# Kernel optimization log

Measured on AMD Instinct MI355X. Metric: run time of the kernel, lower is better.

Reference implementation:

```python
import jax, jax.numpy as jnp
import numpy as np

B, S, D, H = 2, 2048, 1024, 16
DK = D // H


def setup_inputs() -> dict:
    key = jax.random.key(0)
    ks = jax.random.split(key, 11)
    scale = 1.0 / np.sqrt(D)
    inp = {
        "q": jax.random.normal(ks[0], (B, S, D), jnp.float32),
        "k": jax.random.normal(ks[1], (B, S, D), jnp.float32),
        "v": jax.random.normal(ks[2], (B, S, D), jnp.float32),
        # causal mask, broadcastable to (B, H, S, S); 0 = masked
        "mask": jnp.tril(jnp.ones((S, S), jnp.int32))[None, None, :, :],
        "wq": jax.random.normal(ks[3], (D, D), jnp.float32) * scale,
        "bq": jax.random.normal(ks[4], (D,), jnp.float32) * scale,
        "wk": jax.random.normal(ks[5], (D, D), jnp.float32) * scale,
        "bk": jax.random.normal(ks[6], (D,), jnp.float32) * scale,
        "wv": jax.random.normal(ks[7], (D, D), jnp.float32) * scale,
        "bv": jax.random.normal(ks[8], (D,), jnp.float32) * scale,
        "wo": jax.random.normal(ks[9], (D, D), jnp.float32) * scale,
        "bo": jax.random.normal(ks[10], (D,), jnp.float32) * scale,
    }
    return inp


def reference(q, k, v, mask, wq, bq, wk, bk, wv, bv, wo, bo):
    # Linear projections (torch Linear: y = x @ W^T + b)
    Q = jnp.einsum('bsd,ed->bse', q, wq) + bq
    K = jnp.einsum('bsd,ed->bse', k, wk) + bk
    V = jnp.einsum('bsd,ed->bse', v, wv) + bv
    # split heads -> (B, H, S, d_k)
    Q = Q.reshape(B, S, H, DK).transpose(0, 2, 1, 3)
    K = K.reshape(B, S, H, DK).transpose(0, 2, 1, 3)
    V = V.reshape(B, S, H, DK).transpose(0, 2, 1, 3)
    # naive full-score attention, faithful to the source
    scores = jnp.einsum('bhqd,bhkd->bhqk', Q, K) / jnp.sqrt(jnp.float32(DK))
    scores = jnp.where(mask == 0, -jnp.inf, scores)
    attn = jax.nn.softmax(scores, axis=-1)
    out = jnp.einsum('bhqk,bhkd->bhqd', attn, V)
    # merge heads -> (B, S, D)
    out = out.transpose(0, 2, 1, 3).reshape(B, S, D)
    return jnp.einsum('bsd,ed->bse', out, wo) + bo
```

## Files before the change

### kernel.cpp

```cpp
#include <hip/hip_runtime.h>
#include <hip/hip_bf16.h>
#include <cstdint>

constexpr int Bc = 2, Sc = 2048, Dc = 1024, Hc = 16;
constexpr int Mtok = Bc * Sc;

typedef __bf16 bf16;
typedef __bf16 bf16x4 __attribute__((ext_vector_type(4)));
typedef __bf16 bf16x8 __attribute__((ext_vector_type(8)));
typedef float  f32x4  __attribute__((ext_vector_type(4)));

__device__ __forceinline__ void gld_lds16(const bf16* g, bf16* l) {
  __builtin_amdgcn_global_load_lds(
      (__attribute__((address_space(1))) void*)(void*)g,
      (__attribute__((address_space(3))) void*)l, 16, 0, 0);
}

__global__ __launch_bounds__(256) void convert_all(
    const float* __restrict__ q, const float* __restrict__ k,
    const float* __restrict__ v, const float* __restrict__ wq,
    const float* __restrict__ wk, const float* __restrict__ wv,
    const float* __restrict__ wo, bf16* __restrict__ ws)
{
  constexpr size_t NQ = (size_t)Mtok * Dc;
  constexpr size_t NW = (size_t)Dc * Dc;
  const size_t e = ((size_t)blockIdx.x * 256 + threadIdx.x) * 8;
  const float* src; bf16* dst;
  if (e < 3 * NQ) {
    src = (e < NQ) ? q + e : (e < 2 * NQ) ? k + (e - NQ) : v + (e - 2 * NQ);
    dst = ws + e;
  } else {
    const size_t w = e - 3 * NQ;
    const float* wsrc = (w < NW) ? wq : (w < 2 * NW) ? wk : (w < 3 * NW) ? wv : wo;
    src = wsrc + (w & (NW - 1));
    dst = ws + 5 * NQ + w;
  }
  f32x4 a = ((const f32x4*)src)[0];
  f32x4 b = ((const f32x4*)src)[1];
  bf16x8 t;
  t[0]=(bf16)a[0]; t[1]=(bf16)a[1]; t[2]=(bf16)a[2]; t[3]=(bf16)a[3];
  t[4]=(bf16)b[0]; t[5]=(bf16)b[1]; t[6]=(bf16)b[2]; t[7]=(bf16)b[3];
  *(bf16x8*)dst = t;
}

__global__ __launch_bounds__(256, 6) void gemm_qkv(
    const bf16* __restrict__ Aq, const bf16* __restrict__ Ak,
    const bf16* __restrict__ Av, const bf16* __restrict__ Wb,
    const float* __restrict__ bq, const float* __restrict__ bk,
    const float* __restrict__ bv,
    bf16* __restrict__ Yq, bf16* __restrict__ Yk, bf16* __restrict__ Vt)
{
  __shared__ __attribute__((aligned(16))) bf16 As[64 * 64];
  __shared__ __attribute__((aligned(16))) bf16 Bs[128 * 64];

  const int z = blockIdx.z;
  const bf16*  A    = (z == 0) ? Aq : (z == 1) ? Ak : Av;
  const bf16*  Wz   = Wb + (size_t)z * Dc * Dc;
  const float* bias = (z == 0) ? bq : (z == 1) ? bk : bv;

  const int m0 = blockIdx.x * 64, n0 = blockIdx.y * 128;
  const int tid = threadIdx.x, wave = tid >> 6, lane = tid & 63;
  const int quad = lane >> 4, l16 = lane & 15;
  const int swz = l16 & 7;
  const int sr  = lane >> 3;
  const int scol = ((lane & 7) ^ sr) * 8;

  f32x4 acc[4][2] = {};

  for (int k0 = 0; k0 < Dc; k0 += 64) {
#pragma unroll
    for (int j = 0; j < 2; ++j)
      gld_lds16(A + (size_t)(m0 + wave * 16 + j * 8 + sr) * Dc + k0 + scol,
                &As[(wave * 16 + j * 8) * 64]);
#pragma unroll
    for (int j = 0; j < 4; ++j)
      gld_lds16(Wz + (size_t)(n0 + wave * 32 + j * 8 + sr) * Dc + k0 + scol,
                &Bs[(wave * 32 + j * 8) * 64]);
    __syncthreads();
#pragma unroll
    for (int ks = 0; ks < 2; ++ks) {
      const int pc = ((ks * 4 + quad) ^ swz) * 8;
      bf16x8 af[4];
#pragma unroll
      for (int rt = 0; rt < 4; ++rt)
        af[rt] = *(const bf16x8*)&As[(rt * 16 + l16) * 64 + pc];
#pragma unroll
      for (int ct = 0; ct < 2; ++ct) {
        bf16x8 bfr = *(const bf16x8*)&Bs[(wave * 32 + ct * 16 + l16) * 64 + pc];
#pragma unroll
        for (int rt = 0; rt < 4; ++rt)
          acc[rt][ct] = __builtin_amdgcn_mfma_f32_16x16x32_bf16(af[rt], bfr, acc[rt][ct], 0, 0, 0);
      }
    }
    __syncthreads();
  }

  if (z < 2) {
    bf16* Y = (z == 0) ? Yq : Yk;
#pragma unroll
    for (int ct = 0; ct < 2; ++ct) {
      const int col = n0 + wave * 32 + ct * 16 + l16;
      const float bvv = bias[col];
#pragma unroll
      for (int rt = 0; rt < 4; ++rt)
#pragma unroll
        for (int i = 0; i < 4; ++i) {
          const int row = m0 + rt * 16 + quad * 4 + i;
          Y[(size_t)row * Dc + col] = (bf16)(acc[rt][ct][i] + bvv);
        }
    }
  } else {
#pragma unroll
    for (int ct = 0; ct < 2; ++ct) {
      const int col = n0 + wave * 32 + ct * 16 + l16;
      const float bvv = bias[col];
#pragma unroll
      for (int rt = 0; rt < 4; ++rt) {
        const int row0 = m0 + rt * 16 + quad * 4;
        const int bb = row0 >> 11, s0 = row0 & 2047;
        bf16x4 pk;
#pragma unroll
        for (int i = 0; i < 4; ++i) pk[i] = (bf16)(acc[rt][ct][i] + bvv);
        *(bf16x4*)&Vt[((size_t)bb * Dc + col) * Sc + s0] = pk;
      }
    }
  }
}

__global__ __launch_bounds__(256, 4) void gemm_o(
    const bf16* __restrict__ A, const bf16* __restrict__ Wz,
    const float* __restrict__ bias, float* __restrict__ Y)
{
  __shared__ __attribute__((aligned(16))) bf16 As[64 * 64];
  __shared__ __attribute__((aligned(16))) bf16 Bs[64 * 64];

  const int m0 = blockIdx.x * 64, n0 = blockIdx.y * 64;
  const int tid = threadIdx.x, wave = tid >> 6, lane = tid & 63;
  const int quad = lane >> 4, l16 = lane & 15;
  const int swz = l16 & 7;
  const int sr  = lane >> 3;
  const int scol = ((lane & 7) ^ sr) * 8;

  f32x4 acc[4] = {};

  for (int k0 = 0; k0 < Dc; k0 += 64) {
#pragma unroll
    for (int j = 0; j < 2; ++j) {
      gld_lds16(A  + (size_t)(m0 + wave * 16 + j * 8 + sr) * Dc + k0 + scol,
                &As[(wave * 16 + j * 8) * 64]);
      gld_lds16(Wz + (size_t)(n0 + wave * 16 + j * 8 + sr) * Dc + k0 + scol,
                &Bs[(wave * 16 + j * 8) * 64]);
    }
    __syncthreads();
#pragma unroll
    for (int ks = 0; ks < 2; ++ks) {
      const int pc = ((ks * 4 + quad) ^ swz) * 8;
      bf16x8 bfr = *(const bf16x8*)&Bs[(wave * 16 + l16) * 64 + pc];
#pragma unroll
      for (int rt = 0; rt < 4; ++rt) {
        bf16x8 af = *(const bf16x8*)&As[(rt * 16 + l16) * 64 + pc];
        acc[rt] = __builtin_amdgcn_mfma_f32_16x16x32_bf16(af, bfr, acc[rt], 0, 0, 0);
      }
    }
    __syncthreads();
  }

  const int col = n0 + wave * 16 + l16;
  const float bvv = bias[col];
#pragma unroll
  for (int rt = 0; rt < 4; ++rt)
#pragma unroll
    for (int i = 0; i < 4; ++i) {
      const int row = m0 + rt * 16 + quad * 4 + i;
      Y[(size_t)row * Dc + col] = acc[rt][i] + bvv;
    }
}

template <bool AF32, bool BF32, bool OUTF32>
__global__ __launch_bounds__(256) void gemm128(
    const void* __restrict__ Av, const void* __restrict__ Bv,
    const float* __restrict__ bias, void* __restrict__ Yv,
    int M, int N, int K)
{
  __shared__ __attribute__((aligned(16))) bf16 As[2][128][40];
  __shared__ __attribute__((aligned(16))) bf16 Bs[2][128][40];

  const int m0 = blockIdx.x * 128, n0 = blockIdx.y * 128;
  const int tid = threadIdx.x, wave = tid >> 6, lane = tid & 63;
  const int quad = lane >> 4, l16 = lane & 15;
  const int rw = wave >> 1, cw = wave & 1;
  const int srow = tid >> 1, sc = (tid & 1) * 16;

  f32x4 acc[4][4] = {};

  auto load = [&](const void* P, bool f32, int r0, int k0, bf16x8& lo, bf16x8& hi) {
    if (f32) {
      const float* s = (const float*)P + (size_t)(r0 + srow) * K + k0 + sc;
      f32x4 a0 = ((const f32x4*)s)[0], a1 = ((const f32x4*)s)[1];
      f32x4 a2 = ((const f32x4*)s)[2], a3 = ((const f32x4*)s)[3];
      lo[0]=(bf16)a0[0]; lo[1]=(bf16)a0[1]; lo[2]=(bf16)a0[2]; lo[3]=(bf16)a0[3];
      lo[4]=(bf16)a1[0]; lo[5]=(bf16)a1[1]; lo[6]=(bf16)a1[2]; lo[7]=(bf16)a1[3];
      hi[0]=(bf16)a2[0]; hi[1]=(bf16)a2[1]; hi[2]=(bf16)a2[2]; hi[3]=(bf16)a2[3];
      hi[4]=(bf16)a3[0]; hi[5]=(bf16)a3[1]; hi[6]=(bf16)a3[2]; hi[7]=(bf16)a3[3];
    } else {
      const bf16* s = (const bf16*)P + (size_t)(r0 + srow) * K + k0 + sc;
      lo = ((const bf16x8*)s)[0]; hi = ((const bf16x8*)s)[1];
    }
  };

  bf16x8 alo, ahi, blo, bhi;
  load(Av, AF32, m0, 0, alo, ahi); load(Bv, BF32, n0, 0, blo, bhi);
  *(bf16x8*)&As[0][srow][sc] = alo; *(bf16x8*)&As[0][srow][sc + 8] = ahi;
  *(bf16x8*)&Bs[0][srow][sc] = blo; *(bf16x8*)&Bs[0][srow][sc + 8] = bhi;

  const int NIT = K >> 5;
  for (int it = 0; it < NIT; ++it) {
    __syncthreads();
    const int cur = it & 1;
    const bool pf = (it + 1) < NIT;
    if (pf) { load(Av, AF32, m0, (it+1)*32, alo, ahi); load(Bv, BF32, n0, (it+1)*32, blo, bhi); }

    bf16x8 af[4];
#pragma unroll
    for (int rt = 0; rt < 4; ++rt)
      af[rt] = *(const bf16x8*)&As[cur][rw * 64 + rt * 16 + l16][quad * 8];
#pragma unroll
    for (int ct = 0; ct < 4; ++ct) {
      bf16x8 bfr = *(const bf16x8*)&Bs[cur][cw * 64 + ct * 16 + l16][quad * 8];
#pragma unroll
      for (int rt = 0; rt < 4; ++rt)
        acc[rt][ct] = __builtin_amdgcn_mfma_f32_16x16x32_bf16(af[rt], bfr, acc[rt][ct], 0, 0, 0);
    }
    if (pf) {
      const int nxt = cur ^ 1;
      *(bf16x8*)&As[nxt][srow][sc] = alo; *(bf16x8*)&As[nxt][srow][sc + 8] = ahi;
      *(bf16x8*)&Bs[nxt][srow][sc] = blo; *(bf16x8*)&Bs[nxt][srow][sc + 8] = bhi;
    }
  }

#pragma unroll
  for (int ct = 0; ct < 4; ++ct) {
    const int col = n0 + cw * 64 + ct * 16 + l16;
    const float bvv = bias[col];
#pragma unroll
    for (int rt = 0; rt < 4; ++rt)
#pragma unroll
      for (int i = 0; i < 4; ++i) {
        const int row = m0 + rw * 64 + rt * 16 + quad * 4 + i;
        const float vv = acc[rt][ct][i] + bvv;
        if constexpr (OUTF32) ((float*)Yv)[(size_t)row * N + col] = vv;
        else                  ((bf16*)Yv)[(size_t)row * N + col] = (bf16)vv;
      }
  }
}

__global__ __launch_bounds__(256) void transpose_v(
    const bf16* __restrict__ in, bf16* __restrict__ out)
{
  __shared__ __attribute__((aligned(16))) bf16 tile[64][72];
  const int s0 = blockIdx.x * 64, d0 = blockIdx.y * 64, b = blockIdx.z;
  const int t = threadIdx.x, r = t >> 2, c = (t & 3) * 16;

  const bf16* src = in + (size_t)(b * Sc + s0 + r) * Dc + d0 + c;
  *(bf16x8*)&tile[r][c]     = ((const bf16x8*)src)[0];
  *(bf16x8*)&tile[r][c + 8] = ((const bf16x8*)src)[1];
  __syncthreads();

  bf16x8 t0, t1;
#pragma unroll
  for (int j = 0; j < 8; ++j) t0[j] = tile[c + j][r];
#pragma unroll
  for (int j = 0; j < 8; ++j) t1[j] = tile[c + 8 + j][r];
  bf16* dst = out + (size_t)(b * Dc + d0 + r) * Sc + s0 + c;
  ((bf16x8*)dst)[0] = t0;
  ((bf16x8*)dst)[1] = t1;
}

__global__ __launch_bounds__(256, 6) void attn5(
    const bf16* __restrict__ Q, const bf16* __restrict__ K,
    const bf16* __restrict__ Vt, bf16* __restrict__ O)
{
  __shared__ __attribute__((aligned(16))) bf16 Ks[64 * 64];
  __shared__ __attribute__((aligned(16))) bf16 Vs[64 * 64];
  __shared__ __attribute__((aligned(16))) bf16 Ps[4][16][68];

  const int bh = blockIdx.x, b = bh >> 4, h = bh & 15;
  const int qy = blockIdx.y;
  const int qt = (qy & 8) ? ((qy & 24) | (7 - (qy & 7))) : qy;
  const int q0 = qt * 64;
  const int nkb = qt + 1;

  const int tid = threadIdx.x, wave = tid >> 6, lane = tid & 63;
  const int quad = lane >> 4, l16 = lane & 15;
  const int swz = l16 & 7;
  const int sr  = lane >> 3;
  const int sgc = ((lane & 7) ^ sr) * 8;

  const bf16 onec = (bf16)1.0f;
  const bf16x8 ones = {onec, onec, onec, onec, onec, onec, onec, onec};

  const bf16* qrow = Q + (size_t)(b * Sc + q0 + wave * 16 + l16) * Dc + h * 64 + quad * 8;
  const bf16x8 aq0 = *(const bf16x8*)qrow;
  const bf16x8 aq1 = *(const bf16x8*)(qrow + 32);

  f32x4 oacc[4] = {{0,0,0,0},{0,0,0,0},{0,0,0,0},{0,0,0,0}};
  f32x4 lacc = {0, 0, 0, 0};

  for (int kb = 0; kb < nkb; ++kb) {
    __syncthreads();
#pragma unroll
    for (int j = 0; j < 2; ++j) {
      const int r = wave * 16 + j * 8 + sr;
      gld_lds16(K  + (size_t)(b * Sc + kb * 64 + r) * Dc + h * 64 + sgc,
                &Ks[(wave * 16 + j * 8) * 64]);
      gld_lds16(Vt + (size_t)(b * Dc + h * 64 + r) * Sc + kb * 64 + sgc,
                &Vs[(wave * 16 + j * 8) * 64]);
    }
    __syncthreads();

    f32x4 s[4] = {{0,0,0,0},{0,0,0,0},{0,0,0,0},{0,0,0,0}};
#pragma unroll
    for (int d2 = 0; d2 < 2; ++d2) {
      const bf16x8 bq = d2 ? aq1 : aq0;
#pragma unroll
      for (int ct = 0; ct < 4; ++ct) {
        bf16x8 ak = *(const bf16x8*)
            &Ks[(ct * 16 + l16) * 64 + (((d2 * 4 + quad) ^ swz) * 8)];
        s[ct] = __builtin_amdgcn_mfma_f32_16x16x32_bf16(ak, bq, s[ct], 0, 0, 0);
      }
    }

    if (kb == nkb - 1) {
      const int qcol = wave * 16 + l16;
#pragma unroll
      for (int ct = 0; ct < 4; ++ct) {
        const int key0 = ct * 16 + quad * 4;
        bf16x4 pk;
#pragma unroll
        for (int i = 0; i < 4; ++i)
          pk[i] = (bf16)((key0 + i > qcol) ? 0.f : __expf(s[ct][i] * 0.125f));
        *(bf16x4*)&Ps[wave][l16][key0] = pk;
      }
    } else {
#pragma unroll
      for (int ct = 0; ct < 4; ++ct) {
        bf16x4 pk;
#pragma unroll
        for (int i = 0; i < 4; ++i) pk[i] = (bf16)__expf(s[ct][i] * 0.125f);
        *(bf16x4*)&Ps[wave][l16][ct * 16 + quad * 4] = pk;
      }
    }

    const bf16x8 ap0 = *(const bf16x8*)&Ps[wave][l16][quad * 8];
    const bf16x8 ap1 = *(const bf16x8*)&Ps[wave][l16][32 + quad * 8];

    lacc = __builtin_amdgcn_mfma_f32_16x16x32_bf16(ap0, ones, lacc, 0, 0, 0);
    lacc = __builtin_amdgcn_mfma_f32_16x16x32_bf16(ap1, ones, lacc, 0, 0, 0);

#pragma unroll
    for (int d2 = 0; d2 < 2; ++d2) {
      const bf16x8 ap = d2 ? ap1 : ap0;
#pragma unroll
      for (int ct = 0; ct < 4; ++ct) {
        bf16x8 bv = *(const bf16x8*)
            &Vs[(ct * 16 + l16) * 64 + (((d2 * 4 + quad) ^ swz) * 8)];
        oacc[ct] = __builtin_amdgcn_mfma_f32_16x16x32_bf16(ap, bv, oacc[ct], 0, 0, 0);
      }
    }
  }

  f32x4 rl;
#pragma unroll
  for (int i = 0; i < 4; ++i) rl[i] = 1.0f / lacc[i];
#pragma unroll
  for (int ct = 0; ct < 4; ++ct)
#pragma unroll
    for (int i = 0; i < 4; ++i)
      O[(size_t)(b * Sc + q0 + wave * 16 + quad * 4 + i) * Dc + h * 64 + ct * 16 + l16] =
          (bf16)(oacc[ct][i] * rl[i]);
}

extern "C" void kernel_launch(void* const* d_in, const int* in_sizes, int n_in,
                              void* d_out, int out_size, void* d_ws, size_t ws_size,
                              hipStream_t stream)
{
  const float* q  = (const float*)d_in[0];
  const float* k  = (const float*)d_in[1];
  const float* v  = (const float*)d_in[2];
  const float* wq = (const float*)d_in[4];
  const float* bq = (const float*)d_in[5];
  const float* wk = (const float*)d_in[6];
  const float* bk = (const float*)d_in[7];
  const float* wv = (const float*)d_in[8];
  const float* bv = (const float*)d_in[9];
  const float* wo = (const float*)d_in[10];
  const float* bo = (const float*)d_in[11];
  float* out = (float*)d_out;

  constexpr size_t NQ = (size_t)Mtok * Dc;
  constexpr size_t NW = (size_t)Dc * Dc;
  bf16* W = (bf16*)d_ws;
  const dim3 ga(Hc * Bc, 32);
  const dim3 gt(Sc / 64, Dc / 64, Bc);

  const bool fancy = ws_size >= (size_t)(6 * NQ + 4 * NW) * 2;
  if (fancy) {
    bf16* xq = W;
    bf16* xk = W + NQ;
    bf16* xv = W + 2 * NQ;
    bf16* Qp = W + 3 * NQ;
    bf16* Kp = W + 4 * NQ;
    bf16* wb = W + 5 * NQ;
    bf16* Vt = W + 5 * NQ + 4 * NW;
    bf16* AO = W;

    convert_all<<<8192, 256, 0, stream>>>(q, k, v, wq, wk, wv, wo, W);
    gemm_qkv<<<dim3(Mtok / 64, Dc / 128, 3), 256, 0, stream>>>(
        xq, xk, xv, wb, bq, bk, bv, Qp, Kp, Vt);
    attn5<<<ga, 256, 0, stream>>>(Qp, Kp, Vt, AO);
    gemm_o<<<dim3(Mtok / 64, Dc / 64), 256, 0, stream>>>(AO, wb + 3 * NW, bo, out);
  } else {
    bf16* Qp = W;
    bf16* Kp = W + NQ;
    bf16* Vp = W + 2 * NQ;
    bf16* Vt = W + 3 * NQ;
    bf16* AO = W + 4 * NQ;
    const dim3 gg(Mtok / 128, Dc / 128);
    gemm128<true, true, false><<<gg, 256, 0, stream>>>(q, wq, bq, Qp, Mtok, Dc, Dc);
    gemm128<true, true, false><<<gg, 256, 0, stream>>>(k, wk, bk, Kp, Mtok, Dc, Dc);
    gemm128<true, true, false><<<gg, 256, 0, stream>>>(v, wv, bv, Vp, Mtok, Dc, Dc);
    transpose_v<<<gt, 256, 0, stream>>>(Vp, Vt);
    attn5<<<ga, 256, 0, stream>>>(Qp, Kp, Vt, AO);
    gemm128<false, true, true><<<gg, 256, 0, stream>>>(AO, wo, bo, out, Mtok, Dc, Dc);
  }
}
```

Before: 216.0 us.

## Double-buffer GEMM and attention tiles, enlarge attention blocks, fold softmax scale into Q

Both projection GEMMs now double-buffer their LDS tiles. The load of the next K-slice is issued before the MFMAs on the current one, and one barrier per iteration is dropped. The attention kernel grows to 512 threads covering 128 query rows, also double-buffers its K/V tiles, and re-derives the causal masking for the last two key blocks. The 1/sqrt(dk) scale moves into the Q projection epilogue so no per-score multiply is needed. Launch-bound occupancy hints are removed, and the doubled LDS footprint may lower occupancy.

After: 225.8 us. 4.5% more time.

```diff
diff --git a/kernel.cpp b/kernel.cpp
--- a/kernel.cpp
+++ b/kernel.cpp
@@ -43,15 +43,15 @@
   *(bf16x8*)dst = t;
 }
 
-__global__ __launch_bounds__(256, 6) void gemm_qkv(
+__global__ __launch_bounds__(256) void gemm_qkv(
     const bf16* __restrict__ Aq, const bf16* __restrict__ Ak,
     const bf16* __restrict__ Av, const bf16* __restrict__ Wb,
     const float* __restrict__ bq, const float* __restrict__ bk,
     const float* __restrict__ bv,
     bf16* __restrict__ Yq, bf16* __restrict__ Yk, bf16* __restrict__ Vt)
 {
-  __shared__ __attribute__((aligned(16))) bf16 As[64 * 64];
-  __shared__ __attribute__((aligned(16))) bf16 Bs[128 * 64];
+  __shared__ __attribute__((aligned(16))) bf16 As[2][64 * 64];
+  __shared__ __attribute__((aligned(16))) bf16 Bs[2][128 * 64];
 
   const int z = blockIdx.z;
   const bf16*  A    = (z == 0) ? Aq : (z == 1) ? Ak : Av;
@@ -65,36 +65,42 @@
   const int sr  = lane >> 3;
   const int scol = ((lane & 7) ^ sr) * 8;
 
-  f32x4 acc[4][2] = {};
-
-  for (int k0 = 0; k0 < Dc; k0 += 64) {
+  auto stage = [&](int buf, int k0) {
 #pragma unroll
     for (int j = 0; j < 2; ++j)
       gld_lds16(A + (size_t)(m0 + wave * 16 + j * 8 + sr) * Dc + k0 + scol,
-                &As[(wave * 16 + j * 8) * 64]);
+                &As[buf][(wave * 16 + j * 8) * 64]);
 #pragma unroll
     for (int j = 0; j < 4; ++j)
       gld_lds16(Wz + (size_t)(n0 + wave * 32 + j * 8 + sr) * Dc + k0 + scol,
-                &Bs[(wave * 32 + j * 8) * 64]);
+                &Bs[buf][(wave * 32 + j * 8) * 64]);
+  };
+
+  f32x4 acc[4][2] = {};
+
+  stage(0, 0);
+  for (int it = 0; it < 16; ++it) {
+    const int cur = it & 1;
     __syncthreads();
+    if (it + 1 < 16) stage(cur ^ 1, (it + 1) * 64);
 #pragma unroll
     for (int ks = 0; ks < 2; ++ks) {
       const int pc = ((ks * 4 + quad) ^ swz) * 8;
       bf16x8 af[4];
 #pragma unroll
       for (int rt = 0; rt < 4; ++rt)
-        af[rt] = *(const bf16x8*)&As[(rt * 16 + l16) * 64 + pc];
+        af[rt] = *(const bf16x8*)&As[cur][(rt * 16 + l16) * 64 + pc];
 #pragma unroll
       for (int ct = 0; ct < 2; ++ct) {
-        bf16x8 bfr = *(const bf16x8*)&Bs[(wave * 32 + ct * 16 + l16) * 64 + pc];
+        bf16x8 bfr = *(const bf16x8*)&Bs[cur][(wave * 32 + ct * 16 + l16) * 64 + pc];
 #pragma unroll
         for (int rt = 0; rt < 4; ++rt)
           acc[rt][ct] = __builtin_amdgcn_mfma_f32_16x16x32_bf16(af[rt], bfr, acc[rt][ct], 0, 0, 0);
       }
     }
-    __syncthreads();
-  }
-
+  }
+
+  const float osc = (z == 0) ? 0.125f : 1.0f;
   if (z < 2) {
     bf16* Y = (z == 0) ? Yq : Yk;
 #pragma unroll
@@ -106,7 +112,7 @@
 #pragma unroll
         for (int i = 0; i < 4; ++i) {
           const int row = m0 + rt * 16 + quad * 4 + i;
-          Y[(size_t)row * Dc + col] = (bf16)(acc[rt][ct][i] + bvv);
+          Y[(size_t)row * Dc + col] = (bf16)((acc[rt][ct][i] + bvv) * osc);
         }
     }
   } else {
@@ -127,12 +133,12 @@
   }
 }
 
-__global__ __launch_bounds__(256, 4) void gemm_o(
+__global__ __launch_bounds__(256) void gemm_o(
     const bf16* __restrict__ A, const bf16* __restrict__ Wz,
     const float* __restrict__ bias, float* __restrict__ Y)
 {
-  __shared__ __attribute__((aligned(16))) bf16 As[64 * 64];
-  __shared__ __attribute__((aligned(16))) bf16 Bs[64 * 64];
+  __shared__ __attribute__((aligned(16))) bf16 As[2][64 * 64];
+  __shared__ __attribute__((aligned(16))) bf16 Bs[2][64 * 64];
 
   const int m0 = blockIdx.x * 64, n0 = blockIdx.y * 64;
   const int tid = threadIdx.x, wave = tid >> 6, lane = tid & 63;
@@ -141,28 +147,33 @@
   const int sr  = lane >> 3;
   const int scol = ((lane & 7) ^ sr) * 8;
 
-  f32x4 acc[4] = {};
-
-  for (int k0 = 0; k0 < Dc; k0 += 64) {
+  auto stage = [&](int buf, int k0) {
 #pragma unroll
     for (int j = 0; j < 2; ++j) {
       gld_lds16(A  + (size_t)(m0 + wave * 16 + j * 8 + sr) * Dc + k0 + scol,
-                &As[(wave * 16 + j * 8) * 64]);
+                &As[buf][(wave * 16 + j * 8) * 64]);
       gld_lds16(Wz + (size_t)(n0 + wave * 16 + j * 8 + sr) * Dc + k0 + scol,
-                &Bs[(wave * 16 + j * 8) * 64]);
-    }
+                &Bs[buf][(wave * 16 + j * 8) * 64]);
+    }
+  };
+
+  f32x4 acc[4] = {};
+
+  stage(0, 0);
+  for (int it = 0; it < 16; ++it) {
+    const int cur = it & 1;
     __syncthreads();
+    if (it + 1 < 16) stage(cur ^ 1, (it + 1) * 64);
 #pragma unroll
     for (int ks = 0; ks < 2; ++ks) {
       const int pc = ((ks * 4 + quad) ^ swz) * 8;
-      bf16x8 bfr = *(const bf16x8*)&Bs[(wave * 16 + l16) * 64 + pc];
+      bf16x8 bfr = *(const bf16x8*)&Bs[cur][(wave * 16 + l16) * 64 + pc];
 #pragma unroll
       for (int rt = 0; rt < 4; ++rt) {
-        bf16x8 af = *(const bf16x8*)&As[(rt * 16 + l16) * 64 + pc];
+        bf16x8 af = *(const bf16x8*)&As[cur][(rt * 16 + l16) * 64 + pc];
         acc[rt] = __builtin_amdgcn_mfma_f32_16x16x32_bf16(af, bfr, acc[rt], 0, 0, 0);
       }
     }
-    __syncthreads();
   }
 
   const int col = n0 + wave * 16 + l16;
@@ -180,7 +191,7 @@
 __global__ __launch_bounds__(256) void gemm128(
     const void* __restrict__ Av, const void* __restrict__ Bv,
     const float* __restrict__ bias, void* __restrict__ Yv,
-    int M, int N, int K)
+    int M, int N, int K, float oscale)
 {
   __shared__ __attribute__((aligned(16))) bf16 As[2][128][40];
   __shared__ __attribute__((aligned(16))) bf16 Bs[2][128][40];
@@ -247,7 +258,7 @@
 #pragma unroll
       for (int i = 0; i < 4; ++i) {
         const int row = m0 + rw * 64 + rt * 16 + quad * 4 + i;
-        const float vv = acc[rt][ct][i] + bvv;
+        const float vv = (acc[rt][ct][i] + bvv) * oscale;
         if constexpr (OUTF32) ((float*)Yv)[(size_t)row * N + col] = vv;
         else                  ((bf16*)Yv)[(size_t)row * N + col] = (bf16)vv;
       }
@@ -276,19 +287,19 @@
   ((bf16x8*)dst)[1] = t1;
 }
 
-__global__ __launch_bounds__(256, 6) void attn5(
+__global__ __launch_bounds__(512, 6) void attn6(
     const bf16* __restrict__ Q, const bf16* __restrict__ K,
     const bf16* __restrict__ Vt, bf16* __restrict__ O)
 {
-  __shared__ __attribute__((aligned(16))) bf16 Ks[64 * 64];
-  __shared__ __attribute__((aligned(16))) bf16 Vs[64 * 64];
-  __shared__ __attribute__((aligned(16))) bf16 Ps[4][16][68];
+  __shared__ __attribute__((aligned(16))) bf16 Ks[2][64 * 64];
+  __shared__ __attribute__((aligned(16))) bf16 Vs[2][64 * 64];
+  __shared__ __attribute__((aligned(16))) bf16 Ps[8][16][68];
 
   const int bh = blockIdx.x, b = bh >> 4, h = bh & 15;
   const int qy = blockIdx.y;
-  const int qt = (qy & 8) ? ((qy & 24) | (7 - (qy & 7))) : qy;
-  const int q0 = qt * 64;
-  const int nkb = qt + 1;
+  const int qt = (qy & 8) ? ((qy & 8) | (7 - (qy & 7))) : qy;
+  const int q0 = qt * 128;
+  const int nkb = 2 * (qt + 1);
 
   const int tid = threadIdx.x, wave = tid >> 6, lane = tid & 63;
   const int quad = lane >> 4, l16 = lane & 15;
@@ -303,20 +314,22 @@
   const bf16x8 aq0 = *(const bf16x8*)qrow;
   const bf16x8 aq1 = *(const bf16x8*)(qrow + 32);
 
+  auto stageKV = [&](int buf, int kb) {
+    const int r = wave * 8 + sr;
+    gld_lds16(K  + (size_t)(b * Sc + kb * 64 + r) * Dc + h * 64 + sgc,
+              &Ks[buf][(wave * 8) * 64]);
+    gld_lds16(Vt + (size_t)(b * Dc + h * 64 + r) * Sc + kb * 64 + sgc,
+              &Vs[buf][(wave * 8) * 64]);
+  };
+
   f32x4 oacc[4] = {{0,0,0,0},{0,0,0,0},{0,0,0,0},{0,0,0,0}};
   f32x4 lacc = {0, 0, 0, 0};
 
+  stageKV(0, 0);
   for (int kb = 0; kb < nkb; ++kb) {
+    const int cur = kb & 1;
     __syncthreads();
-#pragma unroll
-    for (int j = 0; j < 2; ++j) {
-      const int r = wave * 16 + j * 8 + sr;
-      gld_lds16(K  + (size_t)(b * Sc + kb * 64 + r) * Dc + h * 64 + sgc,
-                &Ks[(wave * 16 + j * 8) * 64]);
-      gld_lds16(Vt + (size_t)(b * Dc + h * 64 + r) * Sc + kb * 64 + sgc,
-                &Vs[(wave * 16 + j * 8) * 64]);
-    }
-    __syncthreads();
+    if (kb + 1 < nkb) stageKV(cur ^ 1, kb + 1);
 
     f32x4 s[4] = {{0,0,0,0},{0,0,0,0},{0,0,0,0},{0,0,0,0}};
 #pragma unroll
@@ -325,28 +338,28 @@
 #pragma unroll
       for (int ct = 0; ct < 4; ++ct) {
         bf16x8 ak = *(const bf16x8*)
-            &Ks[(ct * 16 + l16) * 64 + (((d2 * 4 + quad) ^ swz) * 8)];
+            &Ks[cur][(ct * 16 + l16) * 64 + (((d2 * 4 + quad) ^ swz) * 8)];
         s[ct] = __builtin_amdgcn_mfma_f32_16x16x32_bf16(ak, bq, s[ct], 0, 0, 0);
       }
     }
 
-    if (kb == nkb - 1) {
-      const int qcol = wave * 16 + l16;
+    if (kb >= nkb - 2) {
+      const int qrow_g = q0 + wave * 16 + l16;
 #pragma unroll
       for (int ct = 0; ct < 4; ++ct) {
-        const int key0 = ct * 16 + quad * 4;
+        const int key0 = kb * 64 + ct * 16 + quad * 4;
         bf16x4 pk;
 #pragma unroll
         for (int i = 0; i < 4; ++i)
-          pk[i] = (bf16)((key0 + i > qcol) ? 0.f : __expf(s[ct][i] * 0.125f));
-        *(bf16x4*)&Ps[wave][l16][key0] = pk;
+          pk[i] = (bf16)((key0 + i > qrow_g) ? 0.f : __expf(s[ct][i]));
+        *(bf16x4*)&Ps[wave][l16][ct * 16 + quad * 4] = pk;
       }
     } else {
 #pragma unroll
       for (int ct = 0; ct < 4; ++ct) {
         bf16x4 pk;
 #pragma unroll
-        for (int i = 0; i < 4; ++i) pk[i] = (bf16)__expf(s[ct][i] * 0.125f);
+        for (int i = 0; i < 4; ++i) pk[i] = (bf16)__expf(s[ct][i]);
         *(bf16x4*)&Ps[wave][l16][ct * 16 + quad * 4] = pk;
       }
     }
@@ -363,7 +376,7 @@
 #pragma unroll
       for (int ct = 0; ct < 4; ++ct) {
         bf16x8 bv = *(const bf16x8*)
-            &Vs[(ct * 16 + l16) * 64 + (((d2 * 4 + quad) ^ swz) * 8)];
+            &Vs[cur][(ct * 16 + l16) * 64 + (((d2 * 4 + quad) ^ swz) * 8)];
         oacc[ct] = __builtin_amdgcn_mfma_f32_16x16x32_bf16(ap, bv, oacc[ct], 0, 0, 0);
       }
     }
@@ -400,7 +413,7 @@
   constexpr size_t NQ = (size_t)Mtok * Dc;
   constexpr size_t NW = (size_t)Dc * Dc;
   bf16* W = (bf16*)d_ws;
-  const dim3 ga(Hc * Bc, 32);
+  const dim3 ga(Hc * Bc, 16);
   const dim3 gt(Sc / 64, Dc / 64, Bc);
 
   const bool fancy = ws_size >= (size_t)(6 * NQ + 4 * NW) * 2;
@@ -417,7 +430,7 @@
     convert_all<<<8192, 256, 0, stream>>>(q, k, v, wq, wk, wv, wo, W);
     gemm_qkv<<<dim3(Mtok / 64, Dc / 128, 3), 256, 0, stream>>>(
         xq, xk, xv, wb, bq, bk, bv, Qp, Kp, Vt);
-    attn5<<<ga, 256, 0, stream>>>(Qp, Kp, Vt, AO);
+    attn6<<<ga, 512, 0, stream>>>(Qp, Kp, Vt, AO);
     gemm_o<<<dim3(Mtok / 64, Dc / 64), 256, 0, stream>>>(AO, wb + 3 * NW, bo, out);
   } else {
     bf16* Qp = W;
@@ -426,11 +439,11 @@
     bf16* Vt = W + 3 * NQ;
     bf16* AO = W + 4 * NQ;
     const dim3 gg(Mtok / 128, Dc / 128);
-    gemm128<true, true, false><<<gg, 256, 0, stream>>>(q, wq, bq, Qp, Mtok, Dc, Dc);
-    gemm128<true, true, false><<<gg, 256, 0, stream>>>(k, wk, bk, Kp, Mtok, Dc, Dc);
-    gemm128<true, true, false><<<gg, 256, 0, stream>>>(v, wv, bv, Vp, Mtok, Dc, Dc);
+    gemm128<true, true, false><<<gg, 256, 0, stream>>>(q, wq, bq, Qp, Mtok, Dc, Dc, 0.125f);
+    gemm128<true, true, false><<<gg, 256, 0, stream>>>(k, wk, bk, Kp, Mtok, Dc, Dc, 1.0f);
+    gemm128<true, true, false><<<gg, 256, 0, stream>>>(v, wv, bv, Vp, Mtok, Dc, Dc, 1.0f);
     transpose_v<<<gt, 256, 0, stream>>>(Vp, Vt);
-    attn5<<<ga, 256, 0, stream>>>(Qp, Kp, Vt, AO);
-    gemm128<false, true, true><<<gg, 256, 0, stream>>>(AO, wo, bo, out, Mtok, Dc, Dc);
-  }
-}
+    attn6<<<ga, 512, 0, stream>>>(Qp, Kp, Vt, AO);
+    gemm128<false, true, true><<<gg, 256, 0, stream>>>(AO, wo, bo, out, Mtok, Dc, Dc, 1.0f);
+  }
+}
```
